# Performance work log

Measured on AMD Instinct MI355X. Metric: run time of the kernel, lower is better.

Reference implementation:

```python
import jax, jax.numpy as jnp
import numpy as np
from jax import lax

B, CIN, COUT, LAT, H, W, K = 16, 512, 512, 512, 32, 32, 3


def setup_inputs() -> dict:
    key = jax.random.key(0)
    k1, k2, k3, k4 = jax.random.split(key, 4)
    return {
        "x": jax.random.normal(k1, (B, CIN, H, W), jnp.float32),
        "w": jax.random.normal(k2, (B, LAT), jnp.float32),
        "weight": jax.random.normal(k3, (COUT, CIN, K, K), jnp.float32) * 0.05,
        "bias": jnp.zeros((1, COUT, 1, 1), jnp.float32),
        "affine_w": jax.random.normal(k4, (CIN, LAT), jnp.float32) * 0.02,
        "affine_b": jnp.zeros((CIN,), jnp.float32),
    }


def _blur_kernel():
    # make_kernel([1,3,3,1]) * upsample_factor**2 (factor=2)
    k = jnp.array([1.0, 3.0, 3.0, 1.0], jnp.float32)
    k = k[None, :] * k[:, None]
    k = k / k.sum()
    return k * 4.0  # (4, 4)


def reference(x, w, weight, bias, affine_w, affine_b):
    bs = x.shape[0]
    # style: affine(w) + 1  -> (B, Cin)
    s = w @ affine_w.T + affine_b + 1.0
    # per-sample modulated weights (B, Cout, Cin, K, K)
    wm = s[:, None, :, None, None] * weight[None]
    # demodulation
    d = lax.rsqrt(jnp.sum(wm * wm, axis=(2, 3, 4)) + 1e-8)  # (B, Cout)
    wm = d[:, :, None, None, None] * wm
    # fused grouped conv_transpose2d(stride=2, padding=0) expressed as a
    # direct cross-correlation with lhs_dilation=2, pad K-1, spatially
    # flipped per-sample kernels, feature_group_count = batch.
    rhs = jnp.flip(wm, (-2, -1)).reshape(bs * COUT, CIN, K, K)
    xr = x.reshape(1, bs * CIN, H, W)
    y = lax.conv_general_dilated(
        xr, rhs, window_strides=(1, 1),
        padding=((K - 1, K - 1), (K - 1, K - 1)),
        lhs_dilation=(2, 2),
        dimension_numbers=("NCHW", "OIHW", "NCHW"),
        feature_group_count=bs)
    Ho, Wo = y.shape[2], y.shape[3]  # 65, 65
    y = y.reshape(bs, COUT, Ho, Wo)
    # upfirdn2d blur: up=1, down=1, pad=(1,1); torch correlates with the
    # flipped kernel, i.e. a true convolution -> depthwise correlate flipped k.
    bk = jnp.flip(_blur_kernel(), (0, 1))
    dw = jnp.broadcast_to(bk[None, None], (COUT, 1, 4, 4))
    y = lax.conv_general_dilated(
        y, dw, window_strides=(1, 1), padding=((1, 1), (1, 1)),
        dimension_numbers=("NCHW", "OIHW", "NCHW"),
        feature_group_count=COUT)  # -> (B, Cout, 64, 64)
    return y + bias
```

## Files before the change

### kernel.cpp

```cpp
#include <hip/hip_runtime.h>

#define CIN  512
#define COUT 512
#define LAT  512
#define NB   16

typedef __attribute__((ext_vector_type(8))) short bf16x8;
typedef __attribute__((ext_vector_type(4))) float f32x4;

__device__ __forceinline__ unsigned short f2bf(float f) {
    unsigned int u = __builtin_bit_cast(unsigned int, f);
    u += 0x7FFFu + ((u >> 16) & 1u);
    return (unsigned short)(u >> 16);
}

__global__ void k_style(const float* __restrict__ w, const float* __restrict__ aw,
                        const float* __restrict__ ab, float* __restrict__ s) {
    int b = blockIdx.x, ci = threadIdx.x;
    __shared__ float wl[LAT];
    wl[ci] = w[b * LAT + ci];
    __syncthreads();
    const float4* awr = (const float4*)(aw + (size_t)ci * LAT);
    float acc = 0.f;
#pragma unroll 4
    for (int l = 0; l < LAT / 4; ++l) {
        float4 a4 = awr[l];
        const float* wp = &wl[l * 4];
        acc += a4.x * wp[0] + a4.y * wp[1] + a4.z * wp[2] + a4.w * wp[3];
    }
    s[b * CIN + ci] = acc + ab[ci] + 1.0f;
}

__global__ void k_wsq(const float* __restrict__ weight, float* __restrict__ wsq) {
    int co = blockIdx.x, ci = threadIdx.x;
    const float* p = weight + ((size_t)co * CIN + ci) * 9;
    float a = 0.f;
#pragma unroll
    for (int k = 0; k < 9; ++k) a += p[k] * p[k];
    wsq[co * CIN + ci] = a;
}

__global__ void k_demod(const float* __restrict__ s, const float* __restrict__ wsq,
                        float* __restrict__ d) {
    int b = blockIdx.x, co = threadIdx.x;
    __shared__ float s2[CIN];
    float sv = s[b * CIN + co];
    s2[co] = sv * sv;
    __syncthreads();
    const float4* wr = (const float4*)(wsq + (size_t)co * CIN);
    float acc = 0.f;
#pragma unroll 4
    for (int i = 0; i < CIN / 4; ++i) {
        float4 v = wr[i];
        const float* sp = &s2[i * 4];
        acc += v.x * sp[0] + v.y * sp[1] + v.z * sp[2] + v.w * sp[3];
    }
    d[b * COUT + co] = rsqrtf(acc + 1e-8f);
}

__global__ void k_prepw(const float* __restrict__ weight, unsigned short* __restrict__ A9) {
    int co = blockIdx.x, t = threadIdx.x;
    __shared__ float wl[CIN * 9];
    const float* wp = weight + (size_t)co * CIN * 9;
    for (int i = t; i < CIN * 9; i += 256) wl[i] = wp[i];
    __syncthreads();
    unsigned short* ap = A9 + (size_t)co * 9 * CIN;
    for (int i = t; i < CIN * 9; i += 256) {
        int kk = i >> 9, ci = i & 511;
        ap[i] = f2bf(wl[ci * 9 + kk]);
    }
}

__global__ void k_prepx(const float* __restrict__ x, const float* __restrict__ s,
                        unsigned short* __restrict__ XT) {
    int blk = blockIdx.x;
    int b = blk >> 7, pt = (blk >> 3) & 15, ct = blk & 7;
    int p0 = pt * 64, ci0 = ct * 64;
    __shared__ float xt[64][65];
    __shared__ float ss[64];
    int t = threadIdx.x;
    if (t < 64) ss[t] = s[b * CIN + ci0 + t];
    const float* xb = x + ((size_t)(b * CIN + ci0)) * 1024 + p0;
#pragma unroll
    for (int rr = 0; rr < 4; ++rr) {
        int i = rr * 16 + (t >> 4), j = (t & 15) * 4;
        float4 v = *(const float4*)(xb + (size_t)i * 1024 + j);
        xt[i][j] = v.x; xt[i][j + 1] = v.y; xt[i][j + 2] = v.z; xt[i][j + 3] = v.w;
    }
    __syncthreads();
    unsigned short* xo = XT + ((size_t)(b * 1024 + p0)) * CIN + ci0;
#pragma unroll
    for (int rr = 0; rr < 4; ++rr) {
        int jj = rr * 16 + (t >> 4);
        int c4 = (t & 15) * 4;
        ushort4 o;
        o.x = f2bf(xt[c4][jj] * ss[c4]);
        o.y = f2bf(xt[c4 + 1][jj] * ss[c4 + 1]);
        o.z = f2bf(xt[c4 + 2][jj] * ss[c4 + 2]);
        o.w = f2bf(xt[c4 + 3][jj] * ss[c4 + 3]);
        *(ushort4*)(xo + (size_t)jj * CIN + c4) = o;
    }
}

__device__ __forceinline__ void gload16(const void* g, void* l) {
    __builtin_amdgcn_global_load_lds(
        (const __attribute__((address_space(1))) void*)g,
        (__attribute__((address_space(3))) void*)l, 16, 0, 0);
}

__device__ __forceinline__ unsigned int swz_goff(unsigned int o) {
    unsigned int row = o >> 6, kb = o & 63u;
    unsigned int kbx = kb ^ (((row >> 1) & 3u) << 4);
    return row * 1024u + kbx;
}

__launch_bounds__(256, 3)
__global__ void k_gemm(const unsigned short* __restrict__ A9,
                       const unsigned short* __restrict__ XT,
                       _Float16* __restrict__ C, int Ns) {
    __shared__ unsigned short smem[8192];
    const int t = threadIdx.x;
    const int bm = blockIdx.x, bn = blockIdx.y;

    const unsigned int o0 = (unsigned)t * 16u;
    const unsigned int o1 = o0 + 4096u;
    char* lA0 = (char*)smem + ((t >> 6) * 1024);
    char* lA1 = lA0 + 4096;
    char* lB0 = lA0 + 8192;
    char* lB1 = lA1 + 8192;
    const char* gA = (const char*)A9 + (size_t)bm * 128 * 1024;
    const char* gB = (const char*)XT + (size_t)bn * 128 * 1024;
    const char* pA0 = gA + swz_goff(o0);
    const char* pA1 = gA + swz_goff(o1);
    const char* pB0 = gB + swz_goff(o0);
    const char* pB1 = gB + swz_goff(o1);

    const int lane = t & 63, w = t >> 6, wr = w >> 1, wc = w & 1;
    const int lrow = lane & 15;
    const unsigned int kbx = (unsigned)(((lane >> 4) << 4) ^ (((lrow >> 1) & 3) << 4));
    unsigned int offA[4], offB[4];
#pragma unroll
    for (int f = 0; f < 4; ++f) {
        offA[f] = (unsigned)((wr * 64 + f * 16 + lrow) * 64) + kbx;
        offB[f] = 8192u + (unsigned)((wc * 64 + f * 16 + lrow) * 64) + kbx;
    }

    f32x4 acc[4][4];
#pragma unroll
    for (int i = 0; i < 4; ++i)
#pragma unroll
        for (int j = 0; j < 4; ++j) acc[i][j] = (f32x4){0.f, 0.f, 0.f, 0.f};

    for (int it = 0; it < 16; ++it) {
        __syncthreads();
        gload16(pA0, lA0); gload16(pA1, lA1);
        gload16(pB0, lB0); gload16(pB1, lB1);
        pA0 += 64; pA1 += 64; pB0 += 64; pB1 += 64;
        __syncthreads();
        bf16x8 a[4], b[4];
#pragma unroll
        for (int f = 0; f < 4; ++f) a[f] = *(const bf16x8*)((const char*)smem + offA[f]);
#pragma unroll
        for (int f = 0; f < 4; ++f) b[f] = *(const bf16x8*)((const char*)smem + offB[f]);
#pragma unroll
        for (int mf = 0; mf < 4; ++mf)
#pragma unroll
            for (int nf = 0; nf < 4; ++nf)
                acc[mf][nf] = __builtin_amdgcn_mfma_f32_16x16x32_bf16(
                    a[mf], b[nf], acc[mf][nf], 0, 0, 0);
    }

    const int mg0 = bm * 128 + wr * 64 + (lane >> 4) * 4;
    const int ng0 = bn * 128 + wc * 64 + (lane & 15);
#pragma unroll
    for (int mf = 0; mf < 4; ++mf)
#pragma unroll
        for (int j = 0; j < 4; ++j) {
            size_t row = (size_t)(mg0 + mf * 16 + j) * (size_t)Ns;
#pragma unroll
            for (int nf = 0; nf < 4; ++nf)
                C[row + ng0 + nf * 16] = (_Float16)acc[mf][nf][j];
        }
}

__global__ void k_scat(const _Float16* __restrict__ C, const float* __restrict__ dmod,
                       const float* __restrict__ bias, float* __restrict__ out,
                       int b0, int Ns) {
    const int blk = blockIdx.x;
    const int bl = blk >> 9, co = blk & 511, b = b0 + bl;
    const int t = threadIdx.x;
    __shared__ _Float16 ct[9][1024];
    __shared__ float ys[67 * 68];

    const _Float16* Cb = C + (size_t)(co * 9) * (size_t)Ns + bl * 1024;
#pragma unroll
    for (int k = 0; k < 9; ++k)
        ((ushort4*)ct[k])[t] = ((const ushort4*)(Cb + (size_t)k * Ns))[t];
    for (int i = t; i < 67 * 68; i += 256) ys[i] = 0.f;
    __syncthreads();

    for (int id = t; id < 65 * 65; id += 256) {
        int oy = id / 65, ox = id - oy * 65;
        int kys[2], iys[2], nk = 0;
        if (oy & 1) { kys[0] = 1; iys[0] = oy >> 1; nk = 1; }
        else {
            int h = oy >> 1;
            if (h < 32) { kys[0] = 0; iys[0] = h; nk = 1; }
            if (h >= 1) { kys[nk] = 2; iys[nk] = h - 1; nk++; }
        }
        int kxs[2], ixs[2], nx = 0;
        if (ox & 1) { kxs[0] = 1; ixs[0] = ox >> 1; nx = 1; }
        else {
            int h = ox >> 1;
            if (h < 32) { kxs[0] = 0; ixs[0] = h; nx = 1; }
            if (h >= 1) { kxs[nx] = 2; ixs[nx] = h - 1; nx++; }
        }
        float v = 0.f;
        for (int ia = 0; ia < nk; ++ia)
            for (int ic = 0; ic < nx; ++ic)
                v += (float)ct[kys[ia] * 3 + kxs[ic]][iys[ia] * 32 + ixs[ic]];
        ys[(oy + 1) * 68 + ox + 1] = v;
    }
    __syncthreads();

    const float dv = dmod[b * COUT + co];
    const float bv = bias[co];
    const int px = t & 63, py0 = t >> 6;
    float* orow = out + ((size_t)b * COUT + co) * 4096;
    const float kv[4] = {0.25f, 0.75f, 0.75f, 0.25f};
#pragma unroll 4
    for (int j = 0; j < 16; ++j) {
        int py = py0 + 4 * j;
        float sum = 0.f;
#pragma unroll
        for (int u = 0; u < 4; ++u) {
            const float* yr = &ys[(py + u) * 68 + px];
            float rs = yr[0] * kv[0] + yr[1] * kv[1] + yr[2] * kv[2] + yr[3] * kv[3];
            sum = fmaf(rs, kv[u], sum);
        }
        orow[py * 64 + px] = dv * sum + bv;
    }
}

extern "C" void kernel_launch(void* const* d_in, const int* in_sizes, int n_in,
                              void* d_out, int out_size, void* d_ws, size_t ws_size,
                              hipStream_t stream) {
    const float* x      = (const float*)d_in[0];
    const float* w      = (const float*)d_in[1];
    const float* weight = (const float*)d_in[2];
    const float* bias   = (const float*)d_in[3];
    const float* aw     = (const float*)d_in[4];
    const float* ab     = (const float*)d_in[5];
    float* out = (float*)d_out;

    char* wsb = (char*)d_ws;
    float* s            = (float*)wsb;
    float* dmod         = (float*)(wsb + 32768);
    float* wsq          = (float*)(wsb + 65536);
    unsigned short* A9  = (unsigned short*)(wsb + 1114112);
    unsigned short* XT  = (unsigned short*)(wsb + 5832704);
    _Float16* C         = (_Float16*)(wsb + 22609920);
    const size_t cbase  = 22609920;

    size_t avail = ws_size > cbase ? ws_size - cbase : 0;
    int nbc = 16;
    while (nbc > 1 && (size_t)4608 * 1024 * (size_t)nbc * 2 > avail) nbc >>= 1;

    k_style<<<NB, 512, 0, stream>>>(w, aw, ab, s);
    k_wsq<<<COUT, 512, 0, stream>>>(weight, wsq);
    k_demod<<<NB, 512, 0, stream>>>(s, wsq, dmod);
    k_prepw<<<COUT, 256, 0, stream>>>(weight, A9);
    k_prepx<<<2048, 256, 0, stream>>>(x, s, XT);

    const int Ns = nbc * 1024;
    for (int bb = 0; bb < NB; bb += nbc) {
        k_gemm<<<dim3(36, nbc * 8), 256, 0, stream>>>(A9, XT + (size_t)bb * 1024 * CIN, C, Ns);
        k_scat<<<nbc * 512, 256, 0, stream>>>(C, dmod, bias, out, bb, Ns);
    }
}
```

Baseline: 451.7 us.

## Enlarge GEMM tile to 128x256 with 512 threads and restructure scatter-blur kernel

The GEMM now runs 512 threads per block on a 128x256 output tile with a K-step of 64 per iteration, halving the number of barriers and raising reuse of the A tile. The LDS swizzle is adapted to 128-byte rows. The scatter kernel is rewritten to place the nine tap planes into padded fp16 LDS tiles and compute each output parity class directly without per-pixel branching. The 4x4 blur is split into separable horizontal and vertical passes. The intermediate is stored in fp16, which adds rounding risk. Fewer registers per thread may also limit occupancy.

Measured after the change: 459.9 us. No clear change (+1.8%).

```diff
diff --git a/kernel.cpp b/kernel.cpp
--- a/kernel.cpp
+++ b/kernel.cpp
@@ -108,42 +108,43 @@
         (__attribute__((address_space(3))) void*)l, 16, 0, 0);
 }
 
-__device__ __forceinline__ unsigned int swz_goff(unsigned int o) {
-    unsigned int row = o >> 6, kb = o & 63u;
-    unsigned int kbx = kb ^ (((row >> 1) & 3u) << 4);
-    return row * 1024u + kbx;
-}
-
-__launch_bounds__(256, 3)
+__device__ __forceinline__ unsigned swz_off(unsigned o) {
+    unsigned row = o >> 7, kb = o & 127u;
+    return row * 1024u + (kb ^ ((row & 7u) << 4));
+}
+
+__launch_bounds__(512, 4)
 __global__ void k_gemm(const unsigned short* __restrict__ A9,
                        const unsigned short* __restrict__ XT,
                        _Float16* __restrict__ C, int Ns) {
-    __shared__ unsigned short smem[8192];
+    __shared__ unsigned short smem[24576];
     const int t = threadIdx.x;
     const int bm = blockIdx.x, bn = blockIdx.y;
-
-    const unsigned int o0 = (unsigned)t * 16u;
-    const unsigned int o1 = o0 + 4096u;
-    char* lA0 = (char*)smem + ((t >> 6) * 1024);
-    char* lA1 = lA0 + 4096;
-    char* lB0 = lA0 + 8192;
-    char* lB1 = lA1 + 8192;
+    const int w = t >> 6, lane = t & 63;
+    const int wr = w >> 2, wc = w & 3;
+
+    char* sbase = (char*)smem;
+    char* ldsA0 = sbase + w * 1024;
+    char* ldsA1 = ldsA0 + 8192;
+    char* ldsB0 = sbase + 16384 + w * 1024;
+    char* ldsB1 = ldsB0 + 8192;
+    char* ldsB2 = ldsB0 + 16384;
+    char* ldsB3 = ldsB0 + 24576;
+
     const char* gA = (const char*)A9 + (size_t)bm * 128 * 1024;
-    const char* gB = (const char*)XT + (size_t)bn * 128 * 1024;
-    const char* pA0 = gA + swz_goff(o0);
-    const char* pA1 = gA + swz_goff(o1);
-    const char* pB0 = gB + swz_goff(o0);
-    const char* pB1 = gB + swz_goff(o1);
-
-    const int lane = t & 63, w = t >> 6, wr = w >> 1, wc = w & 1;
+    const char* gB = (const char*)XT + (size_t)bn * 256 * 1024;
+    const unsigned to = (unsigned)t * 16u;
+    const unsigned oA0 = swz_off(to), oA1 = swz_off(to + 8192u);
+    const unsigned oB0 = oA0, oB1 = oA1;
+    const unsigned oB2 = swz_off(to + 16384u), oB3 = swz_off(to + 24576u);
+
     const int lrow = lane & 15;
-    const unsigned int kbx = (unsigned)(((lane >> 4) << 4) ^ (((lrow >> 1) & 3) << 4));
-    unsigned int offA[4], offB[4];
-#pragma unroll
-    for (int f = 0; f < 4; ++f) {
-        offA[f] = (unsigned)((wr * 64 + f * 16 + lrow) * 64) + kbx;
-        offB[f] = 8192u + (unsigned)((wc * 64 + f * 16 + lrow) * 64) + kbx;
-    }
+    const unsigned swz = (unsigned)(lane & 7) << 4;
+    const unsigned kg = (unsigned)(lane >> 4) << 4;
+    const unsigned offA_s0 = (unsigned)((wr * 64 + lrow) * 128) + (kg ^ swz);
+    const unsigned offA_s1 = (unsigned)((wr * 64 + lrow) * 128) + ((64u + kg) ^ swz);
+    const unsigned offB_s0 = 16384u + (unsigned)((wc * 64 + lrow) * 128) + (kg ^ swz);
+    const unsigned offB_s1 = 16384u + (unsigned)((wc * 64 + lrow) * 128) + ((64u + kg) ^ swz);
 
     f32x4 acc[4][4];
 #pragma unroll
@@ -151,27 +152,37 @@
 #pragma unroll
         for (int j = 0; j < 4; ++j) acc[i][j] = (f32x4){0.f, 0.f, 0.f, 0.f};
 
-    for (int it = 0; it < 16; ++it) {
+    for (int it = 0; it < 8; ++it) {
         __syncthreads();
-        gload16(pA0, lA0); gload16(pA1, lA1);
-        gload16(pB0, lB0); gload16(pB1, lB1);
-        pA0 += 64; pA1 += 64; pB0 += 64; pB1 += 64;
+        gload16(gA + oA0, ldsA0);
+        gload16(gA + oA1, ldsA1);
+        gload16(gB + oB0, ldsB0);
+        gload16(gB + oB1, ldsB1);
+        gload16(gB + oB2, ldsB2);
+        gload16(gB + oB3, ldsB3);
+        gA += 128; gB += 128;
         __syncthreads();
-        bf16x8 a[4], b[4];
-#pragma unroll
-        for (int f = 0; f < 4; ++f) a[f] = *(const bf16x8*)((const char*)smem + offA[f]);
-#pragma unroll
-        for (int f = 0; f < 4; ++f) b[f] = *(const bf16x8*)((const char*)smem + offB[f]);
-#pragma unroll
-        for (int mf = 0; mf < 4; ++mf)
-#pragma unroll
-            for (int nf = 0; nf < 4; ++nf)
-                acc[mf][nf] = __builtin_amdgcn_mfma_f32_16x16x32_bf16(
-                    a[mf], b[nf], acc[mf][nf], 0, 0, 0);
+        bf16x8 a0[4], a1[4];
+#pragma unroll
+        for (int mf = 0; mf < 4; ++mf) {
+            a0[mf] = *(const bf16x8*)(sbase + offA_s0 + mf * 2048);
+            a1[mf] = *(const bf16x8*)(sbase + offA_s1 + mf * 2048);
+        }
+#pragma unroll
+        for (int nf = 0; nf < 4; ++nf) {
+            bf16x8 b0 = *(const bf16x8*)(sbase + offB_s0 + nf * 2048);
+#pragma unroll
+            for (int mf = 0; mf < 4; ++mf)
+                acc[mf][nf] = __builtin_amdgcn_mfma_f32_16x16x32_bf16(a0[mf], b0, acc[mf][nf], 0, 0, 0);
+            bf16x8 b1 = *(const bf16x8*)(sbase + offB_s1 + nf * 2048);
+#pragma unroll
+            for (int mf = 0; mf < 4; ++mf)
+                acc[mf][nf] = __builtin_amdgcn_mfma_f32_16x16x32_bf16(a1[mf], b1, acc[mf][nf], 0, 0, 0);
+        }
     }
 
     const int mg0 = bm * 128 + wr * 64 + (lane >> 4) * 4;
-    const int ng0 = bn * 128 + wc * 64 + (lane & 15);
+    const int ng0 = bn * 256 + wc * 64 + lrow;
 #pragma unroll
     for (int mf = 0; mf < 4; ++mf)
 #pragma unroll
@@ -189,37 +200,62 @@
     const int blk = blockIdx.x;
     const int bl = blk >> 9, co = blk & 511, b = b0 + bl;
     const int t = threadIdx.x;
-    __shared__ _Float16 ct[9][1024];
-    __shared__ float ys[67 * 68];
+    __shared__ __align__(16) char pool[29648];
+    _Float16* ctp = (_Float16*)pool;
+    _Float16* ysh = (_Float16*)(pool + 20808);
+    float*    hb  = (float*)pool;
+
+    unsigned* zp = (unsigned*)pool;
+    for (int i = t; i < 5202; i += 256) zp[i] = 0u;
+    if (t < 130) { int r = t >> 1, c = (t & 1) * 66; ysh[r * 68 + c] = (_Float16)0.f; }
+    __syncthreads();
 
     const _Float16* Cb = C + (size_t)(co * 9) * (size_t)Ns + bl * 1024;
-#pragma unroll
-    for (int k = 0; k < 9; ++k)
-        ((ushort4*)ct[k])[t] = ((const ushort4*)(Cb + (size_t)k * Ns))[t];
-    for (int i = t; i < 67 * 68; i += 256) ys[i] = 0.f;
-    __syncthreads();
-
-    for (int id = t; id < 65 * 65; id += 256) {
-        int oy = id / 65, ox = id - oy * 65;
-        int kys[2], iys[2], nk = 0;
-        if (oy & 1) { kys[0] = 1; iys[0] = oy >> 1; nk = 1; }
-        else {
-            int h = oy >> 1;
-            if (h < 32) { kys[0] = 0; iys[0] = h; nk = 1; }
-            if (h >= 1) { kys[nk] = 2; iys[nk] = h - 1; nk++; }
-        }
-        int kxs[2], ixs[2], nx = 0;
-        if (ox & 1) { kxs[0] = 1; ixs[0] = ox >> 1; nx = 1; }
-        else {
-            int h = ox >> 1;
-            if (h < 32) { kxs[0] = 0; ixs[0] = h; nx = 1; }
-            if (h >= 1) { kxs[nx] = 2; ixs[nx] = h - 1; nx++; }
-        }
-        float v = 0.f;
-        for (int ia = 0; ia < nk; ++ia)
-            for (int ic = 0; ic < nx; ++ic)
-                v += (float)ct[kys[ia] * 3 + kxs[ic]][iys[ia] * 32 + ixs[ic]];
-        ys[(oy + 1) * 68 + ox + 1] = v;
+    const int px4 = t * 4, liy = px4 >> 5, lix = px4 & 31;
+#pragma unroll
+    for (int k = 0; k < 9; ++k) {
+        ushort4 v = *(const ushort4*)(Cb + (size_t)k * Ns + px4);
+        _Float16* dst = ctp + k * 1156 + (liy + 1) * 34 + lix + 1;
+        dst[0] = __builtin_bit_cast(_Float16, v.x);
+        dst[1] = __builtin_bit_cast(_Float16, v.y);
+        dst[2] = __builtin_bit_cast(_Float16, v.z);
+        dst[3] = __builtin_bit_cast(_Float16, v.w);
+    }
+    __syncthreads();
+
+    {
+        const int a = t >> 3, c0 = t & 7;
+        const _Float16* P = ctp;
+#pragma unroll
+        for (int j = 0; j < 4; ++j) {
+            int c = c0 + 8 * j;
+            ysh[(2 * a + 1) * 68 + 2 * c + 2] = P[4 * 1156 + (a + 1) * 34 + c + 1];
+        }
+        for (int c = c0; c < 33; c += 8)
+            ysh[(2 * a + 1) * 68 + 2 * c + 1] =
+                P[3 * 1156 + (a + 1) * 34 + c + 1] + P[5 * 1156 + (a + 1) * 34 + c];
+        for (int aa = a; aa < 33; aa += 32) {
+#pragma unroll
+            for (int j = 0; j < 4; ++j) {
+                int c = c0 + 8 * j;
+                ysh[(2 * aa) * 68 + 2 * c + 2] =
+                    P[1 * 1156 + (aa + 1) * 34 + c + 1] + P[7 * 1156 + aa * 34 + c + 1];
+            }
+        }
+        for (int aa = a; aa < 33; aa += 32)
+            for (int c = c0; c < 33; c += 8)
+                ysh[(2 * aa) * 68 + 2 * c + 1] =
+                    P[0 * 1156 + (aa + 1) * 34 + c + 1] + P[2 * 1156 + (aa + 1) * 34 + c] +
+                    P[6 * 1156 + aa * 34 + c + 1]       + P[8 * 1156 + aa * 34 + c];
+    }
+    __syncthreads();
+
+    if (t < 128) { int r = (t >> 6) * 66; hb[r * 64 + (t & 63)] = 0.f; }
+    for (int i = t; i < 65 * 64; i += 256) {
+        int oy = i >> 6, px = i & 63;
+        const _Float16* yr = ysh + oy * 68 + px;
+        hb[(oy + 1) * 64 + px] = 0.25f * (float)yr[0] + 0.75f * (float)yr[1] +
+                                 0.75f * (float)yr[2] + 0.25f * (float)yr[3];
     }
     __syncthreads();
 
@@ -227,18 +263,12 @@
     const float bv = bias[co];
     const int px = t & 63, py0 = t >> 6;
     float* orow = out + ((size_t)b * COUT + co) * 4096;
-    const float kv[4] = {0.25f, 0.75f, 0.75f, 0.25f};
-#pragma unroll 4
+#pragma unroll
     for (int j = 0; j < 16; ++j) {
         int py = py0 + 4 * j;
-        float sum = 0.f;
-#pragma unroll
-        for (int u = 0; u < 4; ++u) {
-            const float* yr = &ys[(py + u) * 68 + px];
-            float rs = yr[0] * kv[0] + yr[1] * kv[1] + yr[2] * kv[2] + yr[3] * kv[3];
-            sum = fmaf(rs, kv[u], sum);
-        }
-        orow[py * 64 + px] = dv * sum + bv;
+        const float* hc = hb + py * 64 + px;
+        float sum = 0.25f * hc[0] + 0.75f * hc[64] + 0.75f * hc[128] + 0.25f * hc[192];
+        orow[py * 64 + px] = fmaf(dv, sum, bv);
     }
 }
 
@@ -274,7 +304,7 @@
 
     const int Ns = nbc * 1024;
     for (int bb = 0; bb < NB; bb += nbc) {
-        k_gemm<<<dim3(36, nbc * 8), 256, 0, stream>>>(A9, XT + (size_t)bb * 1024 * CIN, C, Ns);
+        k_gemm<<<dim3(36, nbc * 4), 512, 0, stream>>>(A9, XT + (size_t)bb * 1024 * CIN, C, Ns);
         k_scat<<<nbc * 512, 256, 0, stream>>>(C, dmod, bias, out, bb, Ns);
     }
 }
```
